# Kernel optimization log

Measured on AMD Instinct MI355X. Metric: run time of the kernel, lower is better.

Reference implementation:

```python
import jax, jax.numpy as jnp
import numpy as np

N_FTS = 41024   # HalfKP feature count
HALF = 256      # accumulator half width; FT output is HALF+1 (extra PSQT column)
MAX_FTS = 30    # max active features per side, -1 padded


def setup_inputs() -> dict:
    key = jax.random.key(0)
    ks = jax.random.split(key, 12)
    B = 16384
    wft_ics = jax.random.randint(ks[0], (B, MAX_FTS), 0, N_FTS, dtype=jnp.int32)
    bft_ics = jax.random.randint(ks[1], (B, MAX_FTS), 0, N_FTS, dtype=jnp.int32)
    # emulate -1 padding of inactive feature slots (last 2 slots)
    pad = (jnp.arange(MAX_FTS) >= MAX_FTS - 2)
    wft_ics = jnp.where(pad[None, :], -1, wft_ics)
    bft_ics = jnp.where(pad[None, :], -1, bft_ics)
    stm = jnp.round(jax.random.uniform(ks[2], (B, 1), dtype=jnp.float32))
    ft_w = jax.random.normal(ks[3], (N_FTS, HALF + 1), dtype=jnp.float32) * 0.01
    ft_b = jax.random.normal(ks[4], (HALF + 1,), dtype=jnp.float32) * 0.01
    fc1_w = jax.random.normal(ks[5], (32, 2 * HALF), dtype=jnp.float32) * 0.04
    fc1_b = jax.random.normal(ks[6], (32,), dtype=jnp.float32) * 0.01
    fc2_w = jax.random.normal(ks[7], (32, 32), dtype=jnp.float32) * 0.17
    fc2_b = jax.random.normal(ks[8], (32,), dtype=jnp.float32) * 0.01
    fco_w = jax.random.normal(ks[9], (1, 32), dtype=jnp.float32) * 0.17
    fco_b = jax.random.normal(ks[10], (1,), dtype=jnp.float32) * 0.01
    return {"wft_ics": wft_ics, "bft_ics": bft_ics, "stm": stm,
            "ft_w": ft_w, "ft_b": ft_b, "fc1_w": fc1_w, "fc1_b": fc1_b,
            "fc2_w": fc2_w, "fc2_b": fc2_b, "fco_w": fco_w, "fco_b": fco_b}


def _feature_transform(ics, ft_w, ft_b):
    # sparse gather-and-sum over -1 padded active indices: [B, A] -> [B, HALF+1]
    mask = (ics >= 0)
    safe = jnp.where(mask, ics, 0)
    g = ft_w[safe] * mask[..., None].astype(ft_w.dtype)  # [B, A, HALF+1]
    return g.sum(axis=1) + ft_b


def reference(wft_ics, bft_ics, stm, ft_w, ft_b, fc1_w, fc1_b, fc2_w, fc2_b, fco_w, fco_b):
    wacc = _feature_transform(wft_ics, ft_w, ft_b)
    bacc = _feature_transform(bft_ics, ft_w, ft_b)
    wfts, wpsqt = wacc[:, :HALF], wacc[:, HALF:]
    bfts, bpsqt = bacc[:, :HALF], bacc[:, HALF:]
    x = (1.0 - stm) * jnp.concatenate((wfts, bfts), axis=-1) \
        + stm * jnp.concatenate((bfts, wfts), axis=-1)
    x = jnp.clip(x, 0.0, 1.0)
    x = jnp.clip(x @ fc1_w.T + fc1_b, 0.0, 1.0)
    x = jnp.clip(x @ fc2_w.T + fc2_b, 0.0, 1.0)
    x = x @ fco_w.T + fco_b
    x = x + (wpsqt - bpsqt) * (0.5 - stm)
    return x
```

## Files before the change

kernel.cpp:

```cpp
#include <hip/hip_runtime.h>

#define MAX_FTS 30
#define HALF 256
#define ROWLEN 257

typedef __attribute__((ext_vector_type(4))) _Float16 f16x4;
typedef __attribute__((ext_vector_type(8))) _Float16 f16x8;
typedef __attribute__((ext_vector_type(4))) float    f32x4;

__global__ __launch_bounds__(256) void quant_rows(
    const float* __restrict__ ft_w,
    unsigned char* __restrict__ tbl8,
    float* __restrict__ scl, float* __restrict__ psq, int n_fts)
{
    const int wv = threadIdx.x >> 6, l = threadIdx.x & 63;
    const int r = blockIdx.x * 4 + wv;
    if (r >= n_fts) return;
    const float* row = ft_w + (size_t)r * ROWLEN;

    float v[4];
#pragma unroll
    for (int k = 0; k < 4; ++k) v[k] = row[(l << 2) + k];

    float m = fmaxf(fmaxf(fabsf(v[0]), fabsf(v[1])), fmaxf(fabsf(v[2]), fabsf(v[3])));
#pragma unroll
    for (int d = 1; d < 64; d <<= 1) m = fmaxf(m, __shfl_xor(m, d, 64));

    const float s   = m * (1.0f / 127.0f);
    const float inv = (m > 0.0f) ? (127.0f / m) : 0.0f;

    unsigned int u = 0;
#pragma unroll
    for (int k = 0; k < 4; ++k) {
        int q = (int)rintf(v[k] * inv) + 128;
        u |= ((unsigned int)q & 0xffu) << (8 * k);
    }
    *(unsigned int*)(tbl8 + (size_t)r * 256 + (l << 2)) = u;
    if (l == 0) { scl[r] = s; psq[r] = row[HALF]; }
}

__global__ __launch_bounds__(256) void build_frags(
    const float* __restrict__ fc1_w, const float* __restrict__ fc2_w,
    _Float16* __restrict__ w1f, _Float16* __restrict__ w2f,
    unsigned char* __restrict__ tbl8, float* __restrict__ scl,
    float* __restrict__ psq, int n_fts)
{
    const int idx = blockIdx.x * 256 + threadIdx.x;
    if (idx < 16384) {
        const int nt = idx >> 13, ks = (idx >> 9) & 15, ln = (idx >> 3) & 63, e = idx & 7;
        w1f[idx] = (_Float16)fc1_w[(nt * 16 + (ln & 15)) * 512 + ks * 32 + (ln >> 4) * 8 + e];
    } else if (idx < 16384 + 1024) {
        const int k = idx - 16384;
        const int n2 = k >> 9, ln = (k >> 3) & 63, e = k & 7;
        w2f[k] = (_Float16)fc2_w[(n2 * 16 + (ln & 15)) * 32 + (ln >> 4) * 8 + e];
    } else if (idx < 16384 + 1024 + 64) {
        ((unsigned int*)(tbl8 + (size_t)n_fts * 256))[idx - 17408] = 0x80808080u;
    } else if (idx == 16384 + 1024 + 64) {
        scl[n_fts] = 0.0f; psq[n_fts] = 0.0f;
    }
}

__global__ __launch_bounds__(256) void k1_gather(
    const int* __restrict__ wft, const int* __restrict__ bft,
    const float* __restrict__ stm,
    const unsigned char* __restrict__ tbl8, const float* __restrict__ scl,
    const float* __restrict__ psq, const float* __restrict__ ft_b,
    _Float16* __restrict__ X, float* __restrict__ psterm, int B, int zr)
{
    const int t  = threadIdx.x;
    const int wv = t >> 6;
    const int l  = t & 63;
    const int s  = (blockIdx.x << 2) + wv;
    if (s >= B) return;

    const int lc  = (l < MAX_FTS) ? l : (MAX_FTS - 1);
    const int iwv = wft[s * MAX_FTS + lc];
    const int ibv = bft[s * MAX_FTS + lc];
    const int cwl = (iwv < 0) ? zr : iwv;
    const int cbl = (ibv < 0) ? zr : ibv;

    float swv_ = 0.0f, sbv_ = 0.0f, pv = 0.0f;
    if (l < MAX_FTS) {
        swv_ = scl[cwl];
        sbv_ = scl[cbl];
        pv   = psq[cwl] - psq[cbl];
    }
    const int swi = __builtin_bit_cast(int, swv_);
    const int sbi = __builtin_bit_cast(int, sbv_);

    f32x4 aw = {0.0f, 0.0f, 0.0f, 0.0f};
    f32x4 ab = {0.0f, 0.0f, 0.0f, 0.0f};
    const unsigned char* gb = tbl8 + (l << 2);
#pragma unroll
    for (int i = 0; i < MAX_FTS; ++i) {
        int icw = __builtin_amdgcn_readlane(iwv, i);
        icw = (icw < 0) ? zr : icw;
        const unsigned int qw = *(const unsigned int*)(gb + ((size_t)icw << 8));
        const float sw = __builtin_bit_cast(float, __builtin_amdgcn_readlane(swi, i));
        aw[0] = fmaf(sw, (float)( qw        & 0xffu), aw[0]);
        aw[1] = fmaf(sw, (float)((qw >>  8) & 0xffu), aw[1]);
        aw[2] = fmaf(sw, (float)((qw >> 16) & 0xffu), aw[2]);
        aw[3] = fmaf(sw, (float)( qw >> 24        ), aw[3]);

        int icb = __builtin_amdgcn_readlane(ibv, i);
        icb = (icb < 0) ? zr : icb;
        const unsigned int qb = *(const unsigned int*)(gb + ((size_t)icb << 8));
        const float sb = __builtin_bit_cast(float, __builtin_amdgcn_readlane(sbi, i));
        ab[0] = fmaf(sb, (float)( qb        & 0xffu), ab[0]);
        ab[1] = fmaf(sb, (float)((qb >>  8) & 0xffu), ab[1]);
        ab[2] = fmaf(sb, (float)((qb >> 16) & 0xffu), ab[2]);
        ab[3] = fmaf(sb, (float)( qb >> 24        ), ab[3]);
    }

    float ssw = swv_, ssb = sbv_;
#pragma unroll
    for (int d = 1; d < 64; d <<= 1) {
        ssw += __shfl_xor(ssw, d, 64);
        ssb += __shfl_xor(ssb, d, 64);
        pv  += __shfl_xor(pv,  d, 64);
    }

    const f32x4 fb = *(const f32x4*)(ft_b + (l << 2));
    const float st = stm[s];
    const float os = 1.0f - st;
    const float bw = 128.0f * ssw;
    const float bb = 128.0f * ssb;
    f16x4 hxl, hxh;
#pragma unroll
    for (int k = 0; k < 4; ++k) {
        const float accw = (aw[k] - bw) + fb[k];
        const float accb = (ab[k] - bb) + fb[k];
        float xl = os * accw + st * accb;
        float xh = os * accb + st * accw;
        hxl[k] = (_Float16)fminf(fmaxf(xl, 0.0f), 1.0f);
        hxh[k] = (_Float16)fminf(fmaxf(xh, 0.0f), 1.0f);
    }
    _Float16* xp = X + (size_t)s * 512;
    *(f16x4*)(xp + (l << 2))        = hxl;
    *(f16x4*)(xp + HALF + (l << 2)) = hxh;
    if (l == 0) psterm[s] = pv * (0.5f - st);
}

__global__ __launch_bounds__(256) void k2_mlp(
    const _Float16* __restrict__ X,
    const _Float16* __restrict__ w1f, const _Float16* __restrict__ w2f,
    const float* __restrict__ fc1_b, const float* __restrict__ fc2_b,
    const float* __restrict__ fco_w, const float* __restrict__ fco_b,
    const float* __restrict__ psterm, float* __restrict__ out, int B)
{
    const int t   = threadIdx.x;
    const int wv  = t >> 6;
    const int l   = t & 63;
    const int col = l & 15;
    const int qk  = l >> 4;
    const int s0  = blockIdx.x * 64 + wv * 16;
    if (s0 >= B) return;

    __shared__ __attribute__((aligned(16))) _Float16 h1l[4][16][40];

    f32x4 acc0 = {0.0f, 0.0f, 0.0f, 0.0f};
    f32x4 acc1 = {0.0f, 0.0f, 0.0f, 0.0f};
    const _Float16* xp = X + (size_t)(s0 + col) * 512 + qk * 8;
#pragma unroll
    for (int ks = 0; ks < 16; ++ks) {
        const f16x8 a  = *(const f16x8*)(xp + ks * 32);
        const f16x8 b0 = *(const f16x8*)(w1f + ((size_t)(ks)      * 64 + l) * 8);
        const f16x8 b1 = *(const f16x8*)(w1f + ((size_t)(16 + ks) * 64 + l) * 8);
        acc0 = __builtin_amdgcn_mfma_f32_16x16x32_f16(a, b0, acc0, 0, 0, 0);
        acc1 = __builtin_amdgcn_mfma_f32_16x16x32_f16(a, b1, acc1, 0, 0, 0);
    }

    const float b1a = fc1_b[col], b1b = fc1_b[16 + col];
#pragma unroll
    for (int r = 0; r < 4; ++r) {
        h1l[wv][qk * 4 + r][col]      = (_Float16)fminf(fmaxf(acc0[r] + b1a, 0.0f), 1.0f);
        h1l[wv][qk * 4 + r][16 + col] = (_Float16)fminf(fmaxf(acc1[r] + b1b, 0.0f), 1.0f);
    }
    __builtin_amdgcn_wave_barrier();
    asm volatile("" ::: "memory");

    const f16x8 a2  = *(const f16x8*)(&h1l[wv][col][qk * 8]);
    const f16x8 b20 = *(const f16x8*)(w2f + (size_t)l * 8);
    const f16x8 b21 = *(const f16x8*)(w2f + 512 + (size_t)l * 8);
    f32x4 d0 = {0.0f, 0.0f, 0.0f, 0.0f};
    f32x4 d1 = {0.0f, 0.0f, 0.0f, 0.0f};
    d0 = __builtin_amdgcn_mfma_f32_16x16x32_f16(a2, b20, d0, 0, 0, 0);
    d1 = __builtin_amdgcn_mfma_f32_16x16x32_f16(a2, b21, d1, 0, 0, 0);

    const float b2a = fc2_b[col],  b2b = fc2_b[16 + col];
    const float fwa = fco_w[col],  fwb = fco_w[16 + col];
    float p[4];
#pragma unroll
    for (int r = 0; r < 4; ++r) {
        const float h2a = fminf(fmaxf(d0[r] + b2a, 0.0f), 1.0f);
        const float h2b = fminf(fmaxf(d1[r] + b2b, 0.0f), 1.0f);
        p[r] = h2a * fwa + h2b * fwb;
    }
#pragma unroll
    for (int r = 0; r < 4; ++r) {
        p[r] += __shfl_xor(p[r], 1, 64);
        p[r] += __shfl_xor(p[r], 2, 64);
        p[r] += __shfl_xor(p[r], 4, 64);
        p[r] += __shfl_xor(p[r], 8, 64);
    }
    if (col == 0) {
        const float ob = fco_b[0];
#pragma unroll
        for (int r = 0; r < 4; ++r) {
            const int s = s0 + qk * 4 + r;
            out[s] = p[r] + ob + psterm[s];
        }
    }
}

__global__ __launch_bounds__(256) void nnue_fwd(
    const int* __restrict__ wft, const int* __restrict__ bft,
    const float* __restrict__ stm, const float* __restrict__ ft_w,
    const float* __restrict__ ft_b, const float* __restrict__ fc1_w,
    const float* __restrict__ fc1_b, const float* __restrict__ fc2_w,
    const float* __restrict__ fc2_b, const float* __restrict__ fco_w,
    const float* __restrict__ fco_b, float* __restrict__ out)
{
    const int s = blockIdx.x;
    const int t = threadIdx.x;
    __shared__ int   s_iw[MAX_FTS];
    __shared__ int   s_ib[MAX_FTS];
    __shared__ float s_xx[2 * HALF];
    __shared__ float s_a[32];
    __shared__ float s_b[32];
    __shared__ float s_ps[2];

    if (t < MAX_FTS)                      s_iw[t]      = wft[s * MAX_FTS + t];
    else if (t >= 64 && t < 64 + MAX_FTS) s_ib[t - 64] = bft[s * MAX_FTS + (t - 64)];
    __syncthreads();

    float accw = ft_b[t];
    float accb = ft_b[t];
#pragma unroll
    for (int i = 0; i < MAX_FTS; ++i) {
        int icw = __builtin_amdgcn_readfirstlane(s_iw[i]);
        int icb = __builtin_amdgcn_readfirstlane(s_ib[i]);
        float mw = icw >= 0 ? 1.0f : 0.0f;
        float mb = icb >= 0 ? 1.0f : 0.0f;
        int ow = (icw >= 0 ? icw : 0) * ROWLEN;
        int ob = (icb >= 0 ? icb : 0) * ROWLEN;
        accw = fmaf(ft_w[ow + t], mw, accw);
        accb = fmaf(ft_w[ob + t], mb, accb);
    }
    if (t == 0 || t == 64) {
        const int* idx = (t == 0) ? s_iw : s_ib;
        float ps = 0.0f;
#pragma unroll
        for (int i = 0; i < MAX_FTS; ++i) {
            int ic = idx[i];
            float m = ic >= 0 ? 1.0f : 0.0f;
            int o = (ic >= 0 ? ic : 0) * ROWLEN;
            ps = fmaf(ft_w[o + HALF], m, ps);
        }
        s_ps[t == 0 ? 0 : 1] = ps;
    }
    const float st = stm[s];
    float xl = (1.0f - st) * accw + st * accb;
    float xh = (1.0f - st) * accb + st * accw;
    s_xx[t]        = fminf(fmaxf(xl, 0.0f), 1.0f);
    s_xx[t + HALF] = fminf(fmaxf(xh, 0.0f), 1.0f);
    __syncthreads();

    const int j = t >> 3, p = t & 7;
    const float* w1 = fc1_w + j * (2 * HALF);
    float part = 0.0f;
#pragma unroll
    for (int i = 0; i < 64; ++i) {
        int k = (i << 3) | p;
        part = fmaf(s_xx[k], w1[k], part);
    }
    part += __shfl_xor(part, 1, 64);
    part += __shfl_xor(part, 2, 64);
    part += __shfl_xor(part, 4, 64);
    if (p == 0) s_a[j] = fminf(fmaxf(part + fc1_b[j], 0.0f), 1.0f);
    __syncthreads();

    if (t < 32) {
        float a = fc2_b[t];
        const float* w2 = fc2_w + t * 32;
#pragma unroll
        for (int k = 0; k < 32; ++k) a = fmaf(s_a[k], w2[k], a);
        s_b[t] = fminf(fmaxf(a, 0.0f), 1.0f);
    }
    __syncthreads();

    if (t == 0) {
        float o = fco_b[0];
#pragma unroll
        for (int k = 0; k < 32; ++k) o = fmaf(s_b[k], fco_w[k], o);
        o += (s_ps[0] - s_ps[1]) * (0.5f - st);
        out[s] = o;
    }
}

extern "C" void kernel_launch(void* const* d_in, const int* in_sizes, int n_in,
                              void* d_out, int out_size, void* d_ws, size_t ws_size,
                              hipStream_t stream) {
    const int*   wft   = (const int*)  d_in[0];
    const int*   bft   = (const int*)  d_in[1];
    const float* stm   = (const float*)d_in[2];
    const float* ft_w  = (const float*)d_in[3];
    const float* ft_b  = (const float*)d_in[4];
    const float* fc1_w = (const float*)d_in[5];
    const float* fc1_b = (const float*)d_in[6];
    const float* fc2_w = (const float*)d_in[7];
    const float* fc2_b = (const float*)d_in[8];
    const float* fco_w = (const float*)d_in[9];
    const float* fco_b = (const float*)d_in[10];
    float* out = (float*)d_out;

    const int B     = in_sizes[0] / MAX_FTS;
    const int n_fts = in_sizes[3] / ROWLEN;

    const size_t colpad = (((size_t)(n_fts + 1) * sizeof(float)) + 15) & ~(size_t)15;
    const size_t w1f_b  = 16384 * sizeof(_Float16);
    const size_t w2f_b  = 1024 * sizeof(_Float16);
    const size_t pst_b  = ((size_t)B * sizeof(float) + 15) & ~(size_t)15;
    const size_t x_b    = (size_t)B * 512 * sizeof(_Float16);
    const size_t tbl_b  = (size_t)(n_fts + 1) * 256;
    const size_t need   = 2 * colpad + w1f_b + w2f_b + pst_b + x_b + tbl_b;

    if (ws_size >= need && (B & 63) == 0) {
        char* p = (char*)d_ws;
        float*         scl  = (float*)p;                 p += colpad;
        float*         psq  = (float*)p;                 p += colpad;
        _Float16*      w1f  = (_Float16*)p;              p += w1f_b;
        _Float16*      w2f  = (_Float16*)p;              p += w2f_b;
        float*         pst  = (float*)p;                 p += pst_b;
        _Float16*      X    = (_Float16*)p;              p += x_b;
        unsigned char* tbl8 = (unsigned char*)p;

        quant_rows<<<(n_fts + 3) / 4, 256, 0, stream>>>(ft_w, tbl8, scl, psq, n_fts);
        build_frags<<<69, 256, 0, stream>>>(fc1_w, fc2_w, w1f, w2f, tbl8, scl, psq, n_fts);
        k1_gather<<<(B + 3) / 4, 256, 0, stream>>>(wft, bft, stm, tbl8, scl, psq,
                                                   ft_b, X, pst, B, n_fts);
        k2_mlp<<<B / 64, 256, 0, stream>>>(X, w1f, w2f, fc1_b, fc2_b,
                                           fco_w, fco_b, pst, out, B);
    } else {
        nnue_fwd<<<B, 256, 0, stream>>>(wft, bft, stm, ft_w, ft_b,
                                        fc1_w, fc1_b, fc2_w, fc2_b,
                                        fco_w, fco_b, out);
    }
}
```

Measured before the change: 62.02 us.

## Fuse gather and MLP kernels via shared-memory activations; merge prep kernels

Merges the two weight-preparation kernels into one launch and fuses the sparse feature gather with the MLP. Each 512-thread block now gathers 16 samples (two per wave) into shared memory, then wave 0 runs the MFMA layers. This drops the fp16 X buffer and the psterm round trip through global memory and cuts the launch count from four to two. In exchange, seven of eight waves sit idle during the MLP phase and the block needs a __syncthreads barrier. The larger LDS footprint may also lower occupancy.

New measurement: 56.45 us. -9.0%, faster.

```diff
diff --git a/kernel.cpp b/kernel.cpp
--- a/kernel.cpp
+++ b/kernel.cpp
@@ -8,43 +8,35 @@
 typedef __attribute__((ext_vector_type(8))) _Float16 f16x8;
 typedef __attribute__((ext_vector_type(4))) float    f32x4;
 
-__global__ __launch_bounds__(256) void quant_rows(
-    const float* __restrict__ ft_w,
-    unsigned char* __restrict__ tbl8,
-    float* __restrict__ scl, float* __restrict__ psq, int n_fts)
+__global__ __launch_bounds__(256) void prep(
+    const float* __restrict__ ft_w, const float* __restrict__ fc1_w,
+    const float* __restrict__ fc2_w,
+    unsigned char* __restrict__ tbl8, float* __restrict__ scl,
+    float* __restrict__ psq, _Float16* __restrict__ w1f,
+    _Float16* __restrict__ w2f, int n_fts)
 {
     const int wv = threadIdx.x >> 6, l = threadIdx.x & 63;
     const int r = blockIdx.x * 4 + wv;
-    if (r >= n_fts) return;
-    const float* row = ft_w + (size_t)r * ROWLEN;
-
-    float v[4];
-#pragma unroll
-    for (int k = 0; k < 4; ++k) v[k] = row[(l << 2) + k];
-
-    float m = fmaxf(fmaxf(fabsf(v[0]), fabsf(v[1])), fmaxf(fabsf(v[2]), fabsf(v[3])));
-#pragma unroll
-    for (int d = 1; d < 64; d <<= 1) m = fmaxf(m, __shfl_xor(m, d, 64));
-
-    const float s   = m * (1.0f / 127.0f);
-    const float inv = (m > 0.0f) ? (127.0f / m) : 0.0f;
-
-    unsigned int u = 0;
-#pragma unroll
-    for (int k = 0; k < 4; ++k) {
-        int q = (int)rintf(v[k] * inv) + 128;
-        u |= ((unsigned int)q & 0xffu) << (8 * k);
-    }
-    *(unsigned int*)(tbl8 + (size_t)r * 256 + (l << 2)) = u;
-    if (l == 0) { scl[r] = s; psq[r] = row[HALF]; }
-}
-
-__global__ __launch_bounds__(256) void build_frags(
-    const float* __restrict__ fc1_w, const float* __restrict__ fc2_w,
-    _Float16* __restrict__ w1f, _Float16* __restrict__ w2f,
-    unsigned char* __restrict__ tbl8, float* __restrict__ scl,
-    float* __restrict__ psq, int n_fts)
-{
+    if (r < n_fts) {
+        const float* row = ft_w + (size_t)r * ROWLEN;
+        float v[4];
+#pragma unroll
+        for (int k = 0; k < 4; ++k) v[k] = row[(l << 2) + k];
+        float m = fmaxf(fmaxf(fabsf(v[0]), fabsf(v[1])), fmaxf(fabsf(v[2]), fabsf(v[3])));
+#pragma unroll
+        for (int d = 1; d < 64; d <<= 1) m = fmaxf(m, __shfl_xor(m, d, 64));
+        const float s   = m * (1.0f / 127.0f);
+        const float inv = (m > 0.0f) ? (127.0f / m) : 0.0f;
+        unsigned int u = 0;
+#pragma unroll
+        for (int k = 0; k < 4; ++k) {
+            int q = (int)rintf(v[k] * inv) + 128;
+            u |= ((unsigned int)q & 0xffu) << (8 * k);
+        }
+        *(unsigned int*)(tbl8 + (size_t)r * 256 + (l << 2)) = u;
+        if (l == 0) { scl[r] = s; psq[r] = row[HALF]; }
+    }
+
     const int idx = blockIdx.x * 256 + threadIdx.x;
     if (idx < 16384) {
         const int nt = idx >> 13, ks = (idx >> 9) & 15, ln = (idx >> 3) & 63, e = idx & 7;
@@ -60,110 +52,128 @@
     }
 }
 
-__global__ __launch_bounds__(256) void k1_gather(
+__global__ __launch_bounds__(512) void k_fused(
     const int* __restrict__ wft, const int* __restrict__ bft,
     const float* __restrict__ stm,
     const unsigned char* __restrict__ tbl8, const float* __restrict__ scl,
     const float* __restrict__ psq, const float* __restrict__ ft_b,
-    _Float16* __restrict__ X, float* __restrict__ psterm, int B, int zr)
+    const _Float16* __restrict__ w1f, const _Float16* __restrict__ w2f,
+    const float* __restrict__ fc1_b, const float* __restrict__ fc2_b,
+    const float* __restrict__ fco_w, const float* __restrict__ fco_b,
+    float* __restrict__ out, int zr)
 {
     const int t  = threadIdx.x;
     const int wv = t >> 6;
     const int l  = t & 63;
-    const int s  = (blockIdx.x << 2) + wv;
-    if (s >= B) return;
+    const int s0 = blockIdx.x * 16 + wv * 2;
+    const int s1 = s0 + 1;
+
+    __shared__ __attribute__((aligned(16))) _Float16 Xl[16][520];
+    __shared__ __attribute__((aligned(16))) _Float16 h1l[16][40];
+    __shared__ float ps_l[16];
 
     const int lc  = (l < MAX_FTS) ? l : (MAX_FTS - 1);
-    const int iwv = wft[s * MAX_FTS + lc];
-    const int ibv = bft[s * MAX_FTS + lc];
-    const int cwl = (iwv < 0) ? zr : iwv;
-    const int cbl = (ibv < 0) ? zr : ibv;
-
-    float swv_ = 0.0f, sbv_ = 0.0f, pv = 0.0f;
+    const int iw0 = wft[s0 * MAX_FTS + lc];
+    const int ib0 = bft[s0 * MAX_FTS + lc];
+    const int iw1 = wft[s1 * MAX_FTS + lc];
+    const int ib1 = bft[s1 * MAX_FTS + lc];
+    const int cw0 = (iw0 < 0) ? zr : iw0;
+    const int cb0 = (ib0 < 0) ? zr : ib0;
+    const int cw1 = (iw1 < 0) ? zr : iw1;
+    const int cb1 = (ib1 < 0) ? zr : ib1;
+
+    float sw0_ = 0.0f, sb0_ = 0.0f, pv0 = 0.0f;
+    float sw1_ = 0.0f, sb1_ = 0.0f, pv1 = 0.0f;
     if (l < MAX_FTS) {
-        swv_ = scl[cwl];
-        sbv_ = scl[cbl];
-        pv   = psq[cwl] - psq[cbl];
-    }
-    const int swi = __builtin_bit_cast(int, swv_);
-    const int sbi = __builtin_bit_cast(int, sbv_);
-
-    f32x4 aw = {0.0f, 0.0f, 0.0f, 0.0f};
-    f32x4 ab = {0.0f, 0.0f, 0.0f, 0.0f};
+        sw0_ = scl[cw0]; sb0_ = scl[cb0]; pv0 = psq[cw0] - psq[cb0];
+        sw1_ = scl[cw1]; sb1_ = scl[cb1]; pv1 = psq[cw1] - psq[cb1];
+    }
+    const int sw0i = __builtin_bit_cast(int, sw0_);
+    const int sb0i = __builtin_bit_cast(int, sb0_);
+    const int sw1i = __builtin_bit_cast(int, sw1_);
+    const int sb1i = __builtin_bit_cast(int, sb1_);
+
+    f32x4 aw0 = {0,0,0,0}, ab0 = {0,0,0,0}, aw1 = {0,0,0,0}, ab1 = {0,0,0,0};
     const unsigned char* gb = tbl8 + (l << 2);
+
+#define ACC4(A, u, sc)                                   \
+    A[0] = fmaf(sc, (float)( (u)        & 0xffu), A[0]); \
+    A[1] = fmaf(sc, (float)(((u) >>  8) & 0xffu), A[1]); \
+    A[2] = fmaf(sc, (float)(((u) >> 16) & 0xffu), A[2]); \
+    A[3] = fmaf(sc, (float)( (u) >> 24        ),  A[3]);
+
 #pragma unroll
     for (int i = 0; i < MAX_FTS; ++i) {
-        int icw = __builtin_amdgcn_readlane(iwv, i);
-        icw = (icw < 0) ? zr : icw;
-        const unsigned int qw = *(const unsigned int*)(gb + ((size_t)icw << 8));
-        const float sw = __builtin_bit_cast(float, __builtin_amdgcn_readlane(swi, i));
-        aw[0] = fmaf(sw, (float)( qw        & 0xffu), aw[0]);
-        aw[1] = fmaf(sw, (float)((qw >>  8) & 0xffu), aw[1]);
-        aw[2] = fmaf(sw, (float)((qw >> 16) & 0xffu), aw[2]);
-        aw[3] = fmaf(sw, (float)( qw >> 24        ), aw[3]);
-
-        int icb = __builtin_amdgcn_readlane(ibv, i);
-        icb = (icb < 0) ? zr : icb;
-        const unsigned int qb = *(const unsigned int*)(gb + ((size_t)icb << 8));
-        const float sb = __builtin_bit_cast(float, __builtin_amdgcn_readlane(sbi, i));
-        ab[0] = fmaf(sb, (float)( qb        & 0xffu), ab[0]);
-        ab[1] = fmaf(sb, (float)((qb >>  8) & 0xffu), ab[1]);
-        ab[2] = fmaf(sb, (float)((qb >> 16) & 0xffu), ab[2]);
-        ab[3] = fmaf(sb, (float)( qb >> 24        ), ab[3]);
-    }
-
-    float ssw = swv_, ssb = sbv_;
+        int a = __builtin_amdgcn_readlane(iw0, i); a = (a < 0) ? zr : a;
+        const unsigned int qa = *(const unsigned int*)(gb + ((size_t)a << 8));
+        const float fa = __builtin_bit_cast(float, __builtin_amdgcn_readlane(sw0i, i));
+        ACC4(aw0, qa, fa)
+
+        int b = __builtin_amdgcn_readlane(ib0, i); b = (b < 0) ? zr : b;
+        const unsigned int qb = *(const unsigned int*)(gb + ((size_t)b << 8));
+        const float fb_ = __builtin_bit_cast(float, __builtin_amdgcn_readlane(sb0i, i));
+        ACC4(ab0, qb, fb_)
+
+        int c = __builtin_amdgcn_readlane(iw1, i); c = (c < 0) ? zr : c;
+        const unsigned int qc = *(const unsigned int*)(gb + ((size_t)c << 8));
+        const float fc_ = __builtin_bit_cast(float, __builtin_amdgcn_readlane(sw1i, i));
+        ACC4(aw1, qc, fc_)
+
+        int d = __builtin_amdgcn_readlane(ib1, i); d = (d < 0) ? zr : d;
+        const unsigned int qd = *(const unsigned int*)(gb + ((size_t)d << 8));
+        const float fd = __builtin_bit_cast(float, __builtin_amdgcn_readlane(sb1i, i));
+        ACC4(ab1, qd, fd)
+    }
+#undef ACC4
+
+    float ssw0 = sw0_, ssb0 = sb0_, ssw1 = sw1_, ssb1 = sb1_;
 #pragma unroll
     for (int d = 1; d < 64; d <<= 1) {
-        ssw += __shfl_xor(ssw, d, 64);
-        ssb += __shfl_xor(ssb, d, 64);
-        pv  += __shfl_xor(pv,  d, 64);
+        ssw0 += __shfl_xor(ssw0, d, 64);
+        ssb0 += __shfl_xor(ssb0, d, 64);
+        ssw1 += __shfl_xor(ssw1, d, 64);
+        ssb1 += __shfl_xor(ssb1, d, 64);
+        pv0  += __shfl_xor(pv0,  d, 64);
+        pv1  += __shfl_xor(pv1,  d, 64);
     }
 
     const f32x4 fb = *(const f32x4*)(ft_b + (l << 2));
-    const float st = stm[s];
-    const float os = 1.0f - st;
-    const float bw = 128.0f * ssw;
-    const float bb = 128.0f * ssb;
-    f16x4 hxl, hxh;
+    const float st0 = stm[s0], st1 = stm[s1];
+    const float os0 = 1.0f - st0, os1 = 1.0f - st1;
+    const float bw0 = 128.0f * ssw0, bb0 = 128.0f * ssb0;
+    const float bw1 = 128.0f * ssw1, bb1 = 128.0f * ssb1;
+
+    f16x4 xl0, xh0, xl1, xh1;
 #pragma unroll
     for (int k = 0; k < 4; ++k) {
-        const float accw = (aw[k] - bw) + fb[k];
-        const float accb = (ab[k] - bb) + fb[k];
-        float xl = os * accw + st * accb;
-        float xh = os * accb + st * accw;
-        hxl[k] = (_Float16)fminf(fmaxf(xl, 0.0f), 1.0f);
-        hxh[k] = (_Float16)fminf(fmaxf(xh, 0.0f), 1.0f);
-    }
-    _Float16* xp = X + (size_t)s * 512;
-    *(f16x4*)(xp + (l << 2))        = hxl;
-    *(f16x4*)(xp + HALF + (l << 2)) = hxh;
-    if (l == 0) psterm[s] = pv * (0.5f - st);
-}
-
-__global__ __launch_bounds__(256) void k2_mlp(
-    const _Float16* __restrict__ X,
-    const _Float16* __restrict__ w1f, const _Float16* __restrict__ w2f,
-    const float* __restrict__ fc1_b, const float* __restrict__ fc2_b,
-    const float* __restrict__ fco_w, const float* __restrict__ fco_b,
-    const float* __restrict__ psterm, float* __restrict__ out, int B)
-{
-    const int t   = threadIdx.x;
-    const int wv  = t >> 6;
-    const int l   = t & 63;
+        const float a0 = (aw0[k] - bw0) + fb[k];
+        const float b0 = (ab0[k] - bb0) + fb[k];
+        xl0[k] = (_Float16)fminf(fmaxf(os0 * a0 + st0 * b0, 0.0f), 1.0f);
+        xh0[k] = (_Float16)fminf(fmaxf(os0 * b0 + st0 * a0, 0.0f), 1.0f);
+        const float a1 = (aw1[k] - bw1) + fb[k];
+        const float b1 = (ab1[k] - bb1) + fb[k];
+        xl1[k] = (_Float16)fminf(fmaxf(os1 * a1 + st1 * b1, 0.0f), 1.0f);
+        xh1[k] = (_Float16)fminf(fmaxf(os1 * b1 + st1 * a1, 0.0f), 1.0f);
+    }
+    const int sb0_loc = wv * 2, sb1_loc = wv * 2 + 1;
+    *(f16x4*)(&Xl[sb0_loc][(l << 2)])        = xl0;
+    *(f16x4*)(&Xl[sb0_loc][HALF + (l << 2)]) = xh0;
+    *(f16x4*)(&Xl[sb1_loc][(l << 2)])        = xl1;
+    *(f16x4*)(&Xl[sb1_loc][HALF + (l << 2)]) = xh1;
+    if (l == 0) {
+        ps_l[sb0_loc] = pv0 * (0.5f - st0);
+        ps_l[sb1_loc] = pv1 * (0.5f - st1);
+    }
+    __syncthreads();
+    if (wv != 0) return;
+
     const int col = l & 15;
     const int qk  = l >> 4;
-    const int s0  = blockIdx.x * 64 + wv * 16;
-    if (s0 >= B) return;
-
-    __shared__ __attribute__((aligned(16))) _Float16 h1l[4][16][40];
-
-    f32x4 acc0 = {0.0f, 0.0f, 0.0f, 0.0f};
-    f32x4 acc1 = {0.0f, 0.0f, 0.0f, 0.0f};
-    const _Float16* xp = X + (size_t)(s0 + col) * 512 + qk * 8;
+
+    f32x4 acc0 = {0,0,0,0}, acc1 = {0,0,0,0};
 #pragma unroll
     for (int ks = 0; ks < 16; ++ks) {
-        const f16x8 a  = *(const f16x8*)(xp + ks * 32);
+        const f16x8 a  = *(const f16x8*)(&Xl[col][ks * 32 + qk * 8]);
         const f16x8 b0 = *(const f16x8*)(w1f + ((size_t)(ks)      * 64 + l) * 8);
         const f16x8 b1 = *(const f16x8*)(w1f + ((size_t)(16 + ks) * 64 + l) * 8);
         acc0 = __builtin_amdgcn_mfma_f32_16x16x32_f16(a, b0, acc0, 0, 0, 0);
@@ -173,17 +183,16 @@
     const float b1a = fc1_b[col], b1b = fc1_b[16 + col];
 #pragma unroll
     for (int r = 0; r < 4; ++r) {
-        h1l[wv][qk * 4 + r][col]      = (_Float16)fminf(fmaxf(acc0[r] + b1a, 0.0f), 1.0f);
-        h1l[wv][qk * 4 + r][16 + col] = (_Float16)fminf(fmaxf(acc1[r] + b1b, 0.0f), 1.0f);
+        h1l[qk * 4 + r][col]      = (_Float16)fminf(fmaxf(acc0[r] + b1a, 0.0f), 1.0f);
+        h1l[qk * 4 + r][16 + col] = (_Float16)fminf(fmaxf(acc1[r] + b1b, 0.0f), 1.0f);
     }
     __builtin_amdgcn_wave_barrier();
     asm volatile("" ::: "memory");
 
-    const f16x8 a2  = *(const f16x8*)(&h1l[wv][col][qk * 8]);
+    const f16x8 a2  = *(const f16x8*)(&h1l[col][qk * 8]);
     const f16x8 b20 = *(const f16x8*)(w2f + (size_t)l * 8);
     const f16x8 b21 = *(const f16x8*)(w2f + 512 + (size_t)l * 8);
-    f32x4 d0 = {0.0f, 0.0f, 0.0f, 0.0f};
-    f32x4 d1 = {0.0f, 0.0f, 0.0f, 0.0f};
+    f32x4 d0 = {0,0,0,0}, d1 = {0,0,0,0};
     d0 = __builtin_amdgcn_mfma_f32_16x16x32_f16(a2, b20, d0, 0, 0, 0);
     d1 = __builtin_amdgcn_mfma_f32_16x16x32_f16(a2, b21, d1, 0, 0, 0);
 
@@ -207,8 +216,8 @@
         const float ob = fco_b[0];
 #pragma unroll
         for (int r = 0; r < 4; ++r) {
-            const int s = s0 + qk * 4 + r;
-            out[s] = p[r] + ob + psterm[s];
+            const int sloc = qk * 4 + r;
+            out[blockIdx.x * 16 + sloc] = p[r] + ob + ps_l[sloc];
         }
     }
 }
@@ -320,27 +329,23 @@
     const size_t colpad = (((size_t)(n_fts + 1) * sizeof(float)) + 15) & ~(size_t)15;
     const size_t w1f_b  = 16384 * sizeof(_Float16);
     const size_t w2f_b  = 1024 * sizeof(_Float16);
-    const size_t pst_b  = ((size_t)B * sizeof(float) + 15) & ~(size_t)15;
-    const size_t x_b    = (size_t)B * 512 * sizeof(_Float16);
     const size_t tbl_b  = (size_t)(n_fts + 1) * 256;
-    const size_t need   = 2 * colpad + w1f_b + w2f_b + pst_b + x_b + tbl_b;
-
-    if (ws_size >= need && (B & 63) == 0) {
+    const size_t need   = 2 * colpad + w1f_b + w2f_b + tbl_b;
+
+    const int nbq = (n_fts + 3) / 4;
+
+    if (ws_size >= need && (B & 15) == 0 && nbq >= 69) {
         char* p = (char*)d_ws;
         float*         scl  = (float*)p;                 p += colpad;
         float*         psq  = (float*)p;                 p += colpad;
         _Float16*      w1f  = (_Float16*)p;              p += w1f_b;
         _Float16*      w2f  = (_Float16*)p;              p += w2f_b;
-        float*         pst  = (float*)p;                 p += pst_b;
-        _Float16*      X    = (_Float16*)p;              p += x_b;
         unsigned char* tbl8 = (unsigned char*)p;
 
-        quant_rows<<<(n_fts + 3) / 4, 256, 0, stream>>>(ft_w, tbl8, scl, psq, n_fts);
-        build_frags<<<69, 256, 0, stream>>>(fc1_w, fc2_w, w1f, w2f, tbl8, scl, psq, n_fts);
-        k1_gather<<<(B + 3) / 4, 256, 0, stream>>>(wft, bft, stm, tbl8, scl, psq,
-                                                   ft_b, X, pst, B, n_fts);
-        k2_mlp<<<B / 64, 256, 0, stream>>>(X, w1f, w2f, fc1_b, fc2_b,
-                                           fco_w, fco_b, pst, out, B);
+        prep<<<nbq, 256, 0, stream>>>(ft_w, fc1_w, fc2_w, tbl8, scl, psq, w1f, w2f, n_fts);
+        k_fused<<<B / 16, 512, 0, stream>>>(wft, bft, stm, tbl8, scl, psq, ft_b,
+                                            w1f, w2f, fc1_b, fc2_b, fco_w, fco_b,
+                                            out, n_fts);
     } else {
         nnue_fwd<<<B, 256, 0, stream>>>(wft, bft, stm, ft_w, ft_b,
                                         fc1_w, fc1_b, fc2_w, fc2_b,
```
